# Kernel optimization log

Measured on AMD Instinct MI355X. Metric: run time of the kernel, lower is better.

The kernel has to match this reference:

```python
import jax, jax.numpy as jnp
import numpy as np

L, B, D, H = 2048, 2, 1024, 16
DK = D // H
SCALE = DK ** -0.5


def setup_inputs() -> dict:
    key = jax.random.key(0)
    ks = jax.random.split(key, 11)
    w_std = D ** -0.5
    return {
        "query": jax.random.normal(ks[0], (L, B, D), dtype=jnp.float32),
        "key": jax.random.normal(ks[1], (L, B, D), dtype=jnp.float32),
        "value": jax.random.normal(ks[2], (L, B, D), dtype=jnp.float32),
        "WQ_w": jax.random.normal(ks[3], (D, D), dtype=jnp.float32) * w_std,
        "WQ_b": jnp.zeros((D,), dtype=jnp.float32),
        "WK_w": jax.random.normal(ks[4], (D, D), dtype=jnp.float32) * w_std,
        "WK_b": jnp.zeros((D,), dtype=jnp.float32),
        "WV_w": jax.random.normal(ks[5], (D, D), dtype=jnp.float32) * w_std,
        "WV_b": jnp.zeros((D,), dtype=jnp.float32),
        "WO_w": jax.random.normal(ks[6], (D, D), dtype=jnp.float32) * w_std,
        "WO_b": jnp.zeros((D,), dtype=jnp.float32),
    }


def reference(query, key, value, WQ_w, WQ_b, WK_w, WK_b, WV_w, WV_b, WO_w, WO_b):
    tgt_len, batch, _ = query.shape
    src_len = key.shape[0]
    # linear projections (torch Linear: x @ W^T + b)
    q = (query @ WQ_w.T + WQ_b) * SCALE            # [L, B, D]
    k = key @ WK_w.T + WK_b                        # [S, B, D]
    v = value @ WV_w.T + WV_b                      # [S, B, D]
    # split heads: [len, B, D] -> [B*H, len, DK]
    q = q.reshape(tgt_len, batch * H, DK).transpose(1, 0, 2)
    k = k.reshape(src_len, batch * H, DK).transpose(1, 0, 2)
    v = v.reshape(src_len, batch * H, DK).transpose(1, 0, 2)
    # attention scores and softmax (full [B*H, L, S] matrix, as in the original)
    scores = jnp.einsum('nld,nsd->nls', q, k)      # [B*H, L, S]
    probs = jax.nn.softmax(scores, axis=-1)
    out = jnp.einsum('nls,nsd->nld', probs, v)     # [B*H, L, DK]
    # merge heads: [B*H, L, DK] -> [L, B, D]
    out = out.transpose(1, 0, 2).reshape(tgt_len, batch, D)
    return out @ WO_w.T + WO_b
```

## Files before the change

kernel.cpp:

```cpp
#include <hip/hip_runtime.h>
#include <hip/hip_fp16.h>

#define LL 2048
#define BB 2
#define DD 1024
#define HH 16
#define DKK 64

typedef _Float16 h8 __attribute__((ext_vector_type(8)));
typedef _Float16 h4 __attribute__((ext_vector_type(4)));
typedef float f4 __attribute__((ext_vector_type(4)));
typedef float f16v __attribute__((ext_vector_type(16)));

#define BAR() do {                                              \
    asm volatile("s_waitcnt lgkmcnt(0)" ::: "memory");          \
    __builtin_amdgcn_s_barrier();                               \
    asm volatile("" ::: "memory");                              \
} while (0)

__global__ __launch_bounds__(256) void cvt_w(
    const float* __restrict__ a, const float* __restrict__ b,
    const float* __restrict__ c, const float* __restrict__ d,
    _Float16* __restrict__ ah, _Float16* __restrict__ bh,
    _Float16* __restrict__ ch, _Float16* __restrict__ dh)
{
    const float* src = (blockIdx.y == 0) ? a : (blockIdx.y == 1) ? b
                     : (blockIdx.y == 2) ? c : d;
    _Float16* dst = (blockIdx.y == 0) ? ah : (blockIdx.y == 1) ? bh
                  : (blockIdx.y == 2) ? ch : dh;
    const int i = (blockIdx.x * 256 + threadIdx.x) * 4;
    f4 v = *(const f4*)(src + i);
    h4 o = {(_Float16)v.x, (_Float16)v.y, (_Float16)v.z, (_Float16)v.w};
    *(h4*)(dst + i) = o;
}

__global__ __launch_bounds__(256) void qkv_proj(
    const float* __restrict__ qin, const float* __restrict__ kin,
    const float* __restrict__ vin,
    const _Float16* __restrict__ wq, const float* __restrict__ bq,
    const _Float16* __restrict__ wk, const float* __restrict__ bk,
    const _Float16* __restrict__ wv, const float* __restrict__ bv,
    _Float16* __restrict__ qh, _Float16* __restrict__ kh,
    _Float16* __restrict__ vth)
{
    const int mode = blockIdx.z;
    const float*    X    = (mode == 0) ? qin : (mode == 1) ? kin : vin;
    const _Float16* W    = (mode == 0) ? wq  : (mode == 1) ? wk  : wv;
    const float*    bias = (mode == 0) ? bq  : (mode == 1) ? bk  : bv;

    __shared__ alignas(16) _Float16 a_sm[128][40];
    __shared__ alignas(16) _Float16 b_sm[128][40];

    const int tid  = threadIdx.x;
    const int lane = tid & 63;
    const int wave = tid >> 6;
    const int wm = (wave & 1) * 64;
    const int wn = (wave >> 1) * 64;
    const int m0 = blockIdx.x * 128;
    const int n0 = blockIdx.y * 128;

    const int srow = tid >> 3;
    const int scol = (tid & 7) * 4;
    const int br = tid >> 2;
    const int bc = (tid & 3) * 8;

    f4 acc[4][4];
    #pragma unroll
    for (int i = 0; i < 4; i++)
        #pragma unroll
        for (int j = 0; j < 4; j++)
            #pragma unroll
            for (int r = 0; r < 4; r++) acc[i][j][r] = 0.f;

    const int fr = lane & 15;
    const int fk = (lane >> 4) * 8;

    for (int k0 = 0; k0 < DD; k0 += 32) {
        #pragma unroll
        for (int r = 0; r < 4; r++) {
            f4 va = *(const f4*)(X + (size_t)(m0 + srow + 32 * r) * DD + k0 + scol);
            h4 ha = {(_Float16)va.x, (_Float16)va.y, (_Float16)va.z, (_Float16)va.w};
            *(h4*)&a_sm[srow + 32 * r][scol] = ha;
        }
        *(h8*)&b_sm[br][bc]      = *(const h8*)(W + (size_t)(n0 + br) * DD + k0 + bc);
        *(h8*)&b_sm[64 + br][bc] = *(const h8*)(W + (size_t)(n0 + 64 + br) * DD + k0 + bc);
        __syncthreads();
        h8 af[4], bfr[4];
        #pragma unroll
        for (int i = 0; i < 4; i++) af[i]  = *(const h8*)&a_sm[wm + i * 16 + fr][fk];
        #pragma unroll
        for (int j = 0; j < 4; j++) bfr[j] = *(const h8*)&b_sm[wn + j * 16 + fr][fk];
        #pragma unroll
        for (int i = 0; i < 4; i++)
            #pragma unroll
            for (int j = 0; j < 4; j++)
                acc[i][j] = __builtin_amdgcn_mfma_f32_16x16x32_f16(af[i], bfr[j], acc[i][j], 0, 0, 0);
        __syncthreads();
    }

    const int colc = lane & 15;
    const int rowb = (lane >> 4) * 4;
    #pragma unroll
    for (int i = 0; i < 4; i++) {
        #pragma unroll
        for (int j = 0; j < 4; j++) {
            const int nn = n0 + wn + j * 16 + colc;
            const float bval = bias[nn];
            #pragma unroll
            for (int reg = 0; reg < 4; reg++) {
                const int mm = m0 + wm + i * 16 + rowb + reg;
                float v = acc[i][j][reg] + bval;
                const int b = mm & 1, l = mm >> 1;
                const int h = nn >> 6, dk = nn & 63;
                const int head = b * HH + h;
                if (mode == 0) {
                    v *= 0.125f;
                    qh[((size_t)head * LL + l) * DKK + dk] = (_Float16)v;
                } else if (mode == 1) {
                    kh[((size_t)head * LL + l) * DKK + dk] = (_Float16)v;
                } else {
                    vth[((size_t)head * DKK + dk) * LL + l] = (_Float16)v;
                }
            }
        }
    }
}

__global__ __launch_bounds__(256, 2) void attn(
    const _Float16* __restrict__ qh, const _Float16* __restrict__ kh,
    const _Float16* __restrict__ vth, _Float16* __restrict__ oh)
{
    const int head = blockIdx.y;
    const int q0   = blockIdx.x * 128;
    const int tid = threadIdx.x, lane = tid & 63, wave = tid >> 6;
    const int qw = q0 + wave * 32;

    __shared__ alignas(16) _Float16 k_sm[128][72];
    __shared__ alignas(16) _Float16 vt_sm[64][136];
    __shared__ alignas(16) _Float16 p_sm[4][32][136];

    const int rq = lane & 31;
    const int kb = (lane >> 5) * 8;
    const int tid8 = tid * 8;

    const _Float16* khead  = kh  + (size_t)head * LL * DKK;
    const _Float16* vthead = vth + (size_t)head * DKK * LL;

    const _Float16* qbase = qh + ((size_t)head * LL + qw + rq) * DKK;
    h8 qa[4];
    #pragma unroll
    for (int kf = 0; kf < 4; kf++) qa[kf] = *(const h8*)(qbase + kf * 16 + kb);

    f16v o0, o1;
    float lsum[16];
    #pragma unroll
    for (int r = 0; r < 16; r++) { o0[r] = 0.f; o1[r] = 0.f; lsum[r] = 0.f; }

    #pragma unroll
    for (int t = 0; t < 4; t++) {
        const int flat = t * 2048 + tid8;
        *(h8*)&k_sm[flat >> 6][flat & 63] = *(const h8*)(khead + flat);
        *(h8*)&vt_sm[flat >> 7][flat & 127] =
            *(const h8*)(vthead + (size_t)(flat >> 7) * LL + (flat & 127));
    }
    BAR();

    _Float16* pw = &p_sm[wave][0][0];
    const int prow = 4 * (lane >> 5);

    for (int it = 0; it < 16; ++it) {
        const int s1 = it * 128 + 128;
        const bool more = (s1 < LL);

        h8 kpre[4], vpre[4];
        if (more) {
            const _Float16* kg = khead + (size_t)s1 * DKK;
            #pragma unroll
            for (int t = 0; t < 4; t++) kpre[t] = *(const h8*)(kg + t * 2048 + tid8);
            #pragma unroll
            for (int t = 0; t < 4; t++) {
                const int flat = t * 2048 + tid8;
                vpre[t] = *(const h8*)(vthead + (size_t)(flat >> 7) * LL + s1 + (flat & 127));
            }
        }

        f16v sc[4];
        #pragma unroll
        for (int st = 0; st < 4; st++) {
            #pragma unroll
            for (int r = 0; r < 16; r++) sc[st][r] = 0.f;
            #pragma unroll
            for (int kf = 0; kf < 4; kf++) {
                h8 kf8 = *(const h8*)&k_sm[st * 32 + rq][kf * 16 + kb];
                sc[st] = __builtin_amdgcn_mfma_f32_32x32x16_f16(qa[kf], kf8, sc[st], 0, 0, 0);
            }
        }

        #pragma unroll
        for (int st = 0; st < 4; st++) {
            #pragma unroll
            for (int r = 0; r < 16; r++) {
                float p = __expf(sc[st][r]);
                lsum[r] += p;
                const int row = (r & 3) + 8 * (r >> 2) + prow;
                pw[row * 136 + st * 32 + rq] = (_Float16)p;
            }
        }
        asm volatile("s_waitcnt lgkmcnt(0)" ::: "memory");

        #pragma unroll
        for (int kf2 = 0; kf2 < 8; kf2++) {
            h8 pa = *(const h8*)&pw[rq * 136 + kf2 * 16 + kb];
            h8 b0 = *(const h8*)&vt_sm[rq][kf2 * 16 + kb];
            h8 b1 = *(const h8*)&vt_sm[32 + rq][kf2 * 16 + kb];
            o0 = __builtin_amdgcn_mfma_f32_32x32x16_f16(pa, b0, o0, 0, 0, 0);
            o1 = __builtin_amdgcn_mfma_f32_32x32x16_f16(pa, b1, o1, 0, 0, 0);
        }

        BAR();
        if (more) {
            #pragma unroll
            for (int t = 0; t < 4; t++) {
                const int flat = t * 2048 + tid8;
                *(h8*)&k_sm[flat >> 6][flat & 63] = kpre[t];
            }
            #pragma unroll
            for (int t = 0; t < 4; t++) {
                const int flat = t * 2048 + tid8;
                *(h8*)&vt_sm[flat >> 7][flat & 127] = vpre[t];
            }
            BAR();
        }
    }

    #pragma unroll
    for (int m = 1; m < 32; m <<= 1)
        #pragma unroll
        for (int r = 0; r < 16; r++) lsum[r] += __shfl_xor(lsum[r], m, 64);

    const int b = head >> 4, h = head & 15;
    #pragma unroll
    for (int r = 0; r < 16; r++) {
        const int row = (r & 3) + 8 * (r >> 2) + prow;
        const int ql = qw + row;
        const float inv = 1.0f / lsum[r];
        const size_t base = (size_t)(ql * BB + b) * DD + h * DKK;
        oh[base + rq]      = (_Float16)(o0[r] * inv);
        oh[base + 32 + rq] = (_Float16)(o1[r] * inv);
    }
}

__global__ __launch_bounds__(256) void out_proj(
    const _Float16* __restrict__ oh, const _Float16* __restrict__ wo,
    const float* __restrict__ bo, float* __restrict__ out)
{
    __shared__ alignas(16) _Float16 a_sm[128][40];
    __shared__ alignas(16) _Float16 b_sm[128][40];
    const int tid = threadIdx.x, lane = tid & 63, wave = tid >> 6;
    const int wm = (wave & 1) * 64, wn = (wave >> 1) * 64;
    const int m0 = blockIdx.x * 128, n0 = blockIdx.y * 128;
    const int ar = tid >> 2, ac = (tid & 3) * 8;

    f4 acc[4][4];
    #pragma unroll
    for (int i = 0; i < 4; i++)
        #pragma unroll
        for (int j = 0; j < 4; j++)
            #pragma unroll
            for (int r = 0; r < 4; r++) acc[i][j][r] = 0.f;

    const int fr = lane & 15;
    const int fk = (lane >> 4) * 8;

    for (int k0 = 0; k0 < DD; k0 += 32) {
        *(h8*)&a_sm[ar][ac]      = *(const h8*)(oh + (size_t)(m0 + ar) * DD + k0 + ac);
        *(h8*)&a_sm[64 + ar][ac] = *(const h8*)(oh + (size_t)(m0 + 64 + ar) * DD + k0 + ac);
        *(h8*)&b_sm[ar][ac]      = *(const h8*)(wo + (size_t)(n0 + ar) * DD + k0 + ac);
        *(h8*)&b_sm[64 + ar][ac] = *(const h8*)(wo + (size_t)(n0 + 64 + ar) * DD + k0 + ac);
        __syncthreads();
        h8 af[4], bfr[4];
        #pragma unroll
        for (int i = 0; i < 4; i++) af[i]  = *(const h8*)&a_sm[wm + i * 16 + fr][fk];
        #pragma unroll
        for (int j = 0; j < 4; j++) bfr[j] = *(const h8*)&b_sm[wn + j * 16 + fr][fk];
        #pragma unroll
        for (int i = 0; i < 4; i++)
            #pragma unroll
            for (int j = 0; j < 4; j++)
                acc[i][j] = __builtin_amdgcn_mfma_f32_16x16x32_f16(af[i], bfr[j], acc[i][j], 0, 0, 0);
        __syncthreads();
    }

    const int colc = lane & 15;
    const int rowb = (lane >> 4) * 4;
    #pragma unroll
    for (int i = 0; i < 4; i++) {
        #pragma unroll
        for (int j = 0; j < 4; j++) {
            const int nn = n0 + wn + j * 16 + colc;
            const float bval = bo[nn];
            #pragma unroll
            for (int reg = 0; reg < 4; reg++) {
                const int mm = m0 + wm + i * 16 + rowb + reg;
                out[(size_t)mm * DD + nn] = acc[i][j][reg] + bval;
            }
        }
    }
}

extern "C" void kernel_launch(void* const* d_in, const int* in_sizes, int n_in,
                              void* d_out, int out_size, void* d_ws, size_t ws_size,
                              hipStream_t stream) {
    const float* qin = (const float*)d_in[0];
    const float* kin = (const float*)d_in[1];
    const float* vin = (const float*)d_in[2];
    const float* wq  = (const float*)d_in[3];
    const float* bq  = (const float*)d_in[4];
    const float* wk  = (const float*)d_in[5];
    const float* bk  = (const float*)d_in[6];
    const float* wv  = (const float*)d_in[7];
    const float* bv  = (const float*)d_in[8];
    const float* wo  = (const float*)d_in[9];
    const float* bo  = (const float*)d_in[10];

    const size_t seg = (size_t)32 * LL * DKK;
    _Float16* qh  = (_Float16*)d_ws;
    _Float16* kh  = qh + seg;
    _Float16* vth = kh + seg;
    _Float16* oh  = vth + seg;
    _Float16* wqh = oh + seg;
    _Float16* wkh = wqh + (size_t)DD * DD;
    _Float16* wvh = wkh + (size_t)DD * DD;
    _Float16* woh = wvh + (size_t)DD * DD;

    hipLaunchKernelGGL(cvt_w, dim3(1024, 4), dim3(256), 0, stream,
                       wq, wk, wv, wo, wqh, wkh, wvh, woh);
    hipLaunchKernelGGL(qkv_proj, dim3(32, 8, 3), dim3(256), 0, stream,
                       qin, kin, vin, wqh, bq, wkh, bk, wvh, bv, qh, kh, vth);
    hipLaunchKernelGGL(attn, dim3(16, 32), dim3(256), 0, stream, qh, kh, vth, oh);
    hipLaunchKernelGGL(out_proj, dim3(32, 8), dim3(256), 0, stream, oh, woh,
                       bo, (float*)d_out);
}
```

Measured before the change: 243.5 us.

## Pre-convert inputs to fp16, use direct global-to-LDS loads, exp2 softmax, smaller out tiles

A single conversion kernel now casts the activations to fp16 along with the weights, so the QKV projection can stage tiles with global_load_lds 16-byte transfers straight into unpadded LDS. The softmax scale now folds in log2(e) so the attention kernel can call the hardware exp2 instead of __expf. The output projection uses 64-row tiles to launch twice as many blocks. In exchange there is an extra full pass over the inputs, more workspace, and the unpadded LDS layout may cause bank conflicts on fragment reads.

```diff
diff --git a/kernel.cpp b/kernel.cpp
--- a/kernel.cpp
+++ b/kernel.cpp
@@ -18,25 +18,39 @@
     asm volatile("" ::: "memory");                              \
 } while (0)
 
-__global__ __launch_bounds__(256) void cvt_w(
-    const float* __restrict__ a, const float* __restrict__ b,
-    const float* __restrict__ c, const float* __restrict__ d,
-    _Float16* __restrict__ ah, _Float16* __restrict__ bh,
-    _Float16* __restrict__ ch, _Float16* __restrict__ dh)
+__device__ __forceinline__ void gload_lds16(const void* g, void* l) {
+    __builtin_amdgcn_global_load_lds(
+        (const __attribute__((address_space(1))) void*)g,
+        (__attribute__((address_space(3))) void*)l, 16, 0, 0);
+}
+
+__global__ __launch_bounds__(256) void cvt_all(
+    const float* __restrict__ x0, const float* __restrict__ x1,
+    const float* __restrict__ x2, const float* __restrict__ w0,
+    const float* __restrict__ w1, const float* __restrict__ w2,
+    const float* __restrict__ w3,
+    _Float16* __restrict__ y0, _Float16* __restrict__ y1,
+    _Float16* __restrict__ y2, _Float16* __restrict__ z0,
+    _Float16* __restrict__ z1, _Float16* __restrict__ z2,
+    _Float16* __restrict__ z3)
 {
-    const float* src = (blockIdx.y == 0) ? a : (blockIdx.y == 1) ? b
-                     : (blockIdx.y == 2) ? c : d;
-    _Float16* dst = (blockIdx.y == 0) ? ah : (blockIdx.y == 1) ? bh
-                  : (blockIdx.y == 2) ? ch : dh;
-    const int i = (blockIdx.x * 256 + threadIdx.x) * 4;
-    f4 v = *(const f4*)(src + i);
-    h4 o = {(_Float16)v.x, (_Float16)v.y, (_Float16)v.z, (_Float16)v.w};
-    *(h4*)(dst + i) = o;
+    const int sel = blockIdx.y;
+    if (sel >= 3 && blockIdx.x >= 512) return;
+    const float* src = (sel == 0) ? x0 : (sel == 1) ? x1 : (sel == 2) ? x2
+                     : (sel == 3) ? w0 : (sel == 4) ? w1 : (sel == 5) ? w2 : w3;
+    _Float16* dst = (sel == 0) ? y0 : (sel == 1) ? y1 : (sel == 2) ? y2
+                  : (sel == 3) ? z0 : (sel == 4) ? z1 : (sel == 5) ? z2 : z3;
+    const int i = (blockIdx.x * 256 + threadIdx.x) * 8;
+    f4 a = *(const f4*)(src + i);
+    f4 b = *(const f4*)(src + i + 4);
+    h8 o = {(_Float16)a.x, (_Float16)a.y, (_Float16)a.z, (_Float16)a.w,
+            (_Float16)b.x, (_Float16)b.y, (_Float16)b.z, (_Float16)b.w};
+    *(h8*)(dst + i) = o;
 }
 
 __global__ __launch_bounds__(256) void qkv_proj(
-    const float* __restrict__ qin, const float* __restrict__ kin,
-    const float* __restrict__ vin,
+    const _Float16* __restrict__ xq, const _Float16* __restrict__ xk,
+    const _Float16* __restrict__ xv,
     const _Float16* __restrict__ wq, const float* __restrict__ bq,
     const _Float16* __restrict__ wk, const float* __restrict__ bk,
     const _Float16* __restrict__ wv, const float* __restrict__ bv,
@@ -44,12 +58,12 @@
     _Float16* __restrict__ vth)
 {
     const int mode = blockIdx.z;
-    const float*    X    = (mode == 0) ? qin : (mode == 1) ? kin : vin;
-    const _Float16* W    = (mode == 0) ? wq  : (mode == 1) ? wk  : wv;
-    const float*    bias = (mode == 0) ? bq  : (mode == 1) ? bk  : bv;
-
-    __shared__ alignas(16) _Float16 a_sm[128][40];
-    __shared__ alignas(16) _Float16 b_sm[128][40];
+    const _Float16* X    = (mode == 0) ? xq : (mode == 1) ? xk : xv;
+    const _Float16* W    = (mode == 0) ? wq : (mode == 1) ? wk : wv;
+    const float*    bias = (mode == 0) ? bq : (mode == 1) ? bk : bv;
+
+    __shared__ alignas(16) _Float16 a_sm[128 * 32];
+    __shared__ alignas(16) _Float16 b_sm[128 * 32];
 
     const int tid  = threadIdx.x;
     const int lane = tid & 63;
@@ -59,10 +73,9 @@
     const int m0 = blockIdx.x * 128;
     const int n0 = blockIdx.y * 128;
 
-    const int srow = tid >> 3;
-    const int scol = (tid & 7) * 4;
-    const int br = tid >> 2;
-    const int bc = (tid & 3) * 8;
+    const int srow = tid >> 2;
+    const int scol = (tid & 3) * 8;
+    const int lds_base = wave * 512;
 
     f4 acc[4][4];
     #pragma unroll
@@ -76,20 +89,16 @@
     const int fk = (lane >> 4) * 8;
 
     for (int k0 = 0; k0 < DD; k0 += 32) {
-        #pragma unroll
-        for (int r = 0; r < 4; r++) {
-            f4 va = *(const f4*)(X + (size_t)(m0 + srow + 32 * r) * DD + k0 + scol);
-            h4 ha = {(_Float16)va.x, (_Float16)va.y, (_Float16)va.z, (_Float16)va.w};
-            *(h4*)&a_sm[srow + 32 * r][scol] = ha;
-        }
-        *(h8*)&b_sm[br][bc]      = *(const h8*)(W + (size_t)(n0 + br) * DD + k0 + bc);
-        *(h8*)&b_sm[64 + br][bc] = *(const h8*)(W + (size_t)(n0 + 64 + br) * DD + k0 + bc);
+        gload_lds16(X + (size_t)(m0 + srow) * DD + k0 + scol,       &a_sm[lds_base]);
+        gload_lds16(X + (size_t)(m0 + 64 + srow) * DD + k0 + scol,  &a_sm[2048 + lds_base]);
+        gload_lds16(W + (size_t)(n0 + srow) * DD + k0 + scol,       &b_sm[lds_base]);
+        gload_lds16(W + (size_t)(n0 + 64 + srow) * DD + k0 + scol,  &b_sm[2048 + lds_base]);
         __syncthreads();
         h8 af[4], bfr[4];
         #pragma unroll
-        for (int i = 0; i < 4; i++) af[i]  = *(const h8*)&a_sm[wm + i * 16 + fr][fk];
-        #pragma unroll
-        for (int j = 0; j < 4; j++) bfr[j] = *(const h8*)&b_sm[wn + j * 16 + fr][fk];
+        for (int i = 0; i < 4; i++) af[i]  = *(const h8*)&a_sm[(wm + i * 16 + fr) * 32 + fk];
+        #pragma unroll
+        for (int j = 0; j < 4; j++) bfr[j] = *(const h8*)&b_sm[(wn + j * 16 + fr) * 32 + fk];
         #pragma unroll
         for (int i = 0; i < 4; i++)
             #pragma unroll
@@ -114,7 +123,7 @@
                 const int h = nn >> 6, dk = nn & 63;
                 const int head = b * HH + h;
                 if (mode == 0) {
-                    v *= 0.125f;
+                    v *= 0.1803368801111243f;
                     qh[((size_t)head * LL + l) * DKK + dk] = (_Float16)v;
                 } else if (mode == 1) {
                     kh[((size_t)head * LL + l) * DKK + dk] = (_Float16)v;
@@ -200,7 +209,7 @@
         for (int st = 0; st < 4; st++) {
             #pragma unroll
             for (int r = 0; r < 16; r++) {
-                float p = __expf(sc[st][r]);
+                float p = __builtin_amdgcn_exp2f(sc[st][r]);
                 lsum[r] += p;
                 const int row = (r & 3) + 8 * (r >> 2) + prow;
                 pw[row * 136 + st * 32 + rq] = (_Float16)p;
@@ -254,16 +263,19 @@
     const _Float16* __restrict__ oh, const _Float16* __restrict__ wo,
     const float* __restrict__ bo, float* __restrict__ out)
 {
-    __shared__ alignas(16) _Float16 a_sm[128][40];
-    __shared__ alignas(16) _Float16 b_sm[128][40];
+    __shared__ alignas(16) _Float16 a_sm[64 * 32];
+    __shared__ alignas(16) _Float16 b_sm[128 * 32];
     const int tid = threadIdx.x, lane = tid & 63, wave = tid >> 6;
-    const int wm = (wave & 1) * 64, wn = (wave >> 1) * 64;
-    const int m0 = blockIdx.x * 128, n0 = blockIdx.y * 128;
-    const int ar = tid >> 2, ac = (tid & 3) * 8;
-
-    f4 acc[4][4];
-    #pragma unroll
-    for (int i = 0; i < 4; i++)
+    const int wm = (wave & 1) * 32, wn = (wave >> 1) * 64;
+    const int m0 = blockIdx.x * 64, n0 = blockIdx.y * 128;
+
+    const int srow = tid >> 2;
+    const int scol = (tid & 3) * 8;
+    const int lds_base = wave * 512;
+
+    f4 acc[2][4];
+    #pragma unroll
+    for (int i = 0; i < 2; i++)
         #pragma unroll
         for (int j = 0; j < 4; j++)
             #pragma unroll
@@ -273,18 +285,17 @@
     const int fk = (lane >> 4) * 8;
 
     for (int k0 = 0; k0 < DD; k0 += 32) {
-        *(h8*)&a_sm[ar][ac]      = *(const h8*)(oh + (size_t)(m0 + ar) * DD + k0 + ac);
-        *(h8*)&a_sm[64 + ar][ac] = *(const h8*)(oh + (size_t)(m0 + 64 + ar) * DD + k0 + ac);
-        *(h8*)&b_sm[ar][ac]      = *(const h8*)(wo + (size_t)(n0 + ar) * DD + k0 + ac);
-        *(h8*)&b_sm[64 + ar][ac] = *(const h8*)(wo + (size_t)(n0 + 64 + ar) * DD + k0 + ac);
+        gload_lds16(oh + (size_t)(m0 + srow) * DD + k0 + scol,      &a_sm[lds_base]);
+        gload_lds16(wo + (size_t)(n0 + srow) * DD + k0 + scol,      &b_sm[lds_base]);
+        gload_lds16(wo + (size_t)(n0 + 64 + srow) * DD + k0 + scol, &b_sm[2048 + lds_base]);
         __syncthreads();
-        h8 af[4], bfr[4];
-        #pragma unroll
-        for (int i = 0; i < 4; i++) af[i]  = *(const h8*)&a_sm[wm + i * 16 + fr][fk];
-        #pragma unroll
-        for (int j = 0; j < 4; j++) bfr[j] = *(const h8*)&b_sm[wn + j * 16 + fr][fk];
-        #pragma unroll
-        for (int i = 0; i < 4; i++)
+        h8 af[2], bfr[4];
+        #pragma unroll
+        for (int i = 0; i < 2; i++) af[i]  = *(const h8*)&a_sm[(wm + i * 16 + fr) * 32 + fk];
+        #pragma unroll
+        for (int j = 0; j < 4; j++) bfr[j] = *(const h8*)&b_sm[(wn + j * 16 + fr) * 32 + fk];
+        #pragma unroll
+        for (int i = 0; i < 2; i++)
             #pragma unroll
             for (int j = 0; j < 4; j++)
                 acc[i][j] = __builtin_amdgcn_mfma_f32_16x16x32_f16(af[i], bfr[j], acc[i][j], 0, 0, 0);
@@ -294,7 +305,7 @@
     const int colc = lane & 15;
     const int rowb = (lane >> 4) * 4;
     #pragma unroll
-    for (int i = 0; i < 4; i++) {
+    for (int i = 0; i < 2; i++) {
         #pragma unroll
         for (int j = 0; j < 4; j++) {
             const int nn = n0 + wn + j * 16 + colc;
@@ -332,12 +343,16 @@
     _Float16* wkh = wqh + (size_t)DD * DD;
     _Float16* wvh = wkh + (size_t)DD * DD;
     _Float16* woh = wvh + (size_t)DD * DD;
-
-    hipLaunchKernelGGL(cvt_w, dim3(1024, 4), dim3(256), 0, stream,
-                       wq, wk, wv, wo, wqh, wkh, wvh, woh);
+    _Float16* xqh = woh + (size_t)DD * DD;
+    _Float16* xkh = xqh + seg;
+    _Float16* xvh = xkh + seg;
+
+    hipLaunchKernelGGL(cvt_all, dim3(2048, 7), dim3(256), 0, stream,
+                       qin, kin, vin, wq, wk, wv, wo,
+                       xqh, xkh, xvh, wqh, wkh, wvh, woh);
     hipLaunchKernelGGL(qkv_proj, dim3(32, 8, 3), dim3(256), 0, stream,
-                       qin, kin, vin, wqh, bq, wkh, bk, wvh, bv, qh, kh, vth);
+                       xqh, xkh, xvh, wqh, bq, wkh, bk, wvh, bv, qh, kh, vth);
     hipLaunchKernelGGL(attn, dim3(16, 32), dim3(256), 0, stream, qh, kh, vth, oh);
-    hipLaunchKernelGGL(out_proj, dim3(32, 8), dim3(256), 0, stream, oh, woh,
+    hipLaunchKernelGGL(out_proj, dim3(64, 8), dim3(256), 0, stream, oh, woh,
                        bo, (float*)d_out);
 }
```

Result: faster. 229.9 us (-5.6%).
